# Optimization experiments

Hardware: AMD Instinct MI355X
Metric: run time of the kernel (lower is better)

Reference implementation:

```python
import jax, jax.numpy as jnp
import numpy as np

FRAME_LEN = 128
FFT_LEN = 128            # smallest power of 2 >= frame_length (TF default)
NUM_SPEC_BINS = FFT_LEN // 2 + 1  # 65
NUM_MEL = 80
SAMPLE_RATE = 16000.0
LOWER_HZ, UPPER_HZ = 80.0, 7600.0


def _hz_to_mel(f):
    # TF's HTK-style mel: 1127 * ln(1 + f/700)
    return 1127.0 * np.log1p(np.asarray(f, dtype=np.float64) / 700.0)


def _linear_to_mel_weight_matrix():
    # Faithful port of tf.signal.linear_to_mel_weight_matrix
    linear_freqs = np.linspace(0.0, SAMPLE_RATE / 2.0, NUM_SPEC_BINS)
    spec_mel = _hz_to_mel(linear_freqs[1:])[:, None]            # [64, 1] (bin 0 zeroed)
    edges = np.linspace(_hz_to_mel(LOWER_HZ), _hz_to_mel(UPPER_HZ), NUM_MEL + 2)
    lower, center, upper = edges[None, :-2], edges[None, 1:-1], edges[None, 2:]
    lower_slopes = (spec_mel - lower) / (center - lower)
    upper_slopes = (upper - spec_mel) / (upper - center)
    w = np.maximum(0.0, np.minimum(lower_slopes, upper_slopes))  # [64, 80]
    return np.pad(w, [[1, 0], [0, 0]]).astype(np.float32)        # [65, 80]


_MEL_W = jnp.asarray(_linear_to_mel_weight_matrix())


def setup_inputs() -> dict:
    key = jax.random.key(0)
    x = jax.random.normal(key, (16, 16384), dtype=jnp.float32)
    return {"x": x}


def reference(x):
    B, N = x.shape
    # pad_end=True with frame_step=1 -> N frames, pad FRAME_LEN-1 zeros at the end
    xp = jnp.pad(x, ((0, 0), (0, FRAME_LEN - 1)))
    idx = jnp.arange(N)[:, None] + jnp.arange(FRAME_LEN)[None, :]  # [N, 128]
    frames = xp[:, idx]                                            # [B, N, 128]
    n = jnp.arange(FRAME_LEN, dtype=jnp.float32)
    window = 0.5 - 0.5 * jnp.cos(2.0 * jnp.pi * n / FRAME_LEN)     # periodic Hann
    stft = jnp.fft.rfft(frames * window, n=FFT_LEN, axis=-1)       # [B, N, 65] complex
    mag = jax.lax.stop_gradient(jnp.abs(stft).astype(jnp.float32))
    mel = mag @ _MEL_W                                             # [B, N, 80]
    return jnp.concatenate([x[..., None], mel], axis=-1)           # [B, N, 81]
```

## Files before the change

### kernel.cpp

```cpp
#include <hip/hip_runtime.h>
#include <hip/hip_fp16.h>
#include <math.h>

#define B_SZ 16
#define N_SZ 16384
#define T_FR 64
#define NTHR 256
#define NMEL 80
#define NCH  81

typedef _Float16 h8  __attribute__((ext_vector_type(8)));
typedef _Float16 h4  __attribute__((ext_vector_type(4)));
typedef float    f4  __attribute__((ext_vector_type(4)));
static_assert(sizeof(h8) == 16, "h8 must be 4 VGPRs");

__device__ _Float16 g_tab[2688 * 8];

__global__ void build_tables() {
  const int u = blockIdx.x * blockDim.x + threadIdx.x;
  if (u >= 2688) return;
  const float w0 = 6.2831853071795864769f / 128.0f;
  h8 res;
  if (u < 2048) {
    const int ln = u & 63, kk = (u >> 6) & 3, pol = (u >> 8) & 1, g = u >> 9;
    const int bin = 16 * g + (ln & 15);
    const int k0  = kk * 32 + ((ln >> 4) & 3) * 8;
#pragma unroll
    for (int j = 0; j < 8; ++j) {
      const int k = k0 + j;
      const float wh = 0.5f - 0.5f * __cosf(w0 * (float)k);
      float sv, cv;
      __sincosf(w0 * (float)((bin * k) & 127), &sv, &cv);
      res[j] = (_Float16)(pol ? (-wh * sv) : (wh * cv));
    }
  } else {
    const int u2 = u - 2048;
    const int ln = u2 & 63, kkB = (u2 >> 6) & 1, jt = u2 >> 7;
    const int mj = 16 * jt + (ln & 15);
    const int b0 = kkB * 32 + ((ln >> 4) & 3) * 8;
    const float mlo = 1127.0f * logf(1.0f + 80.0f / 700.0f);
    const float mhi = 1127.0f * logf(1.0f + 7600.0f / 700.0f);
    const float dm  = (mhi - mlo) / 81.0f;
#pragma unroll
    for (int j = 0; j < 8; ++j) {
      const int bin = b0 + j;
      const float m  = 1127.0f * logf(1.0f + 125.0f * (float)bin / 700.0f);
      const float lower = mlo + dm * (float)mj;
      const float ls = (m - lower) / dm;
      const float us = (lower + 2.0f * dm - m) / dm;
      res[j] = (_Float16)fmaxf(0.0f, fminf(ls, us));
    }
  }
  ((h8*)g_tab)[u] = res;
}

__global__ __launch_bounds__(NTHR) void melspec_kernel(const float* __restrict__ x,
                                                       float* __restrict__ out) {
  __shared__ __align__(16) _Float16 xh2[184 * 8];
  __shared__ __align__(16) _Float16 magT[512 * 8];
  __shared__ float xs[64];
  __shared__ __align__(16) float stage[T_FR * NCH];

  const int tid = threadIdx.x;
  const int t0  = blockIdx.x * T_FR;
  const int b   = blockIdx.y;
  const float* xrow = x + (size_t)b * N_SZ;

  const int wv = tid >> 6;
  const int ln = tid & 63;
  const int lr = ln & 15;
  const int lg = (ln >> 4) & 3;

  if (tid < 64) xs[tid] = xrow[t0 + tid];
  if (tid < 184) {
    h8 tmp;
#pragma unroll
    for (int j = 0; j < 8; ++j) {
      const int gix = t0 + tid + j;
      tmp[j] = (_Float16)((gix < N_SZ) ? xrow[gix] : 0.0f);
    }
    *(h8*)(xh2 + tid * 8) = tmp;
  }
  const h8* tabv = (const h8*)g_tab;
  h8 aRe[4], aIm[4];
#pragma unroll
  for (int kk = 0; kk < 4; ++kk) {
    aRe[kk] = tabv[((wv * 2 + 0) * 4 + kk) * 64 + ln];
    aIm[kk] = tabv[((wv * 2 + 1) * 4 + kk) * 64 + ln];
  }
  __syncthreads();

#pragma unroll
  for (int ft = 0; ft < 4; ++ft) {
    f4 cr = {0.f, 0.f, 0.f, 0.f};
    f4 ci = {0.f, 0.f, 0.f, 0.f};
#pragma unroll
    for (int kk = 0; kk < 4; ++kk) {
      const h8 bb = *(const h8*)(xh2 + (16 * ft + 32 * kk + 8 * lg + lr) * 8);
      cr = __builtin_amdgcn_mfma_f32_16x16x32_f16(aRe[kk], bb, cr, 0, 0, 0);
      ci = __builtin_amdgcn_mfma_f32_16x16x32_f16(aIm[kk], bb, ci, 0, 0, 0);
    }
    h4 pk;
#pragma unroll
    for (int v = 0; v < 4; ++v) {
      const float re = cr[v], im = ci[v];
      pk[v] = (_Float16)sqrtf(re * re + im * im);
    }
    const int bg = 2 * wv + (lg >> 1);
    *(h4*)(magT + ((bg * 64 + 16 * ft + lr) * 8 + 4 * (lg & 1))) = pk;
  }
  h8 aW[10];
#pragma unroll
  for (int q = 0; q < 10; ++q) aW[q] = tabv[2048 + q * 64 + ln];
  __syncthreads();

  f4 acc[5];
  {
    const f4 z = {0.f, 0.f, 0.f, 0.f};
#pragma unroll
    for (int i = 0; i < 5; ++i) acc[i] = z;
  }
#pragma unroll
  for (int kkB = 0; kkB < 2; ++kkB) {
    const h8 bb = *(const h8*)(magT + ((kkB * 4 + lg) * 64 + 16 * wv + lr) * 8);
#pragma unroll
    for (int jt = 0; jt < 5; ++jt)
      acc[jt] = __builtin_amdgcn_mfma_f32_16x16x32_f16(aW[jt * 2 + kkB], bb, acc[jt], 0, 0, 0);
  }
  {
    const int fr = 16 * wv + lr;
    float* srow = stage + fr * NCH;
    if (lg == 0) srow[0] = xs[fr];
#pragma unroll
    for (int jt = 0; jt < 5; ++jt)
#pragma unroll
      for (int v = 0; v < 4; ++v)
        srow[1 + 16 * jt + 4 * lg + v] = acc[jt][v];
  }
  __syncthreads();

  float* orow = out + ((size_t)b * N_SZ + t0) * NCH;
#pragma unroll
  for (int i = 0; i < 5; ++i) {
    const int f = i * 1024 + tid * 4;
    *(float4*)(orow + f) = *(const float4*)(stage + f);
  }
  if (tid < 64) orow[5120 + tid] = stage[5120 + tid];
}

extern "C" void kernel_launch(void* const* d_in, const int* in_sizes, int n_in,
                              void* d_out, int out_size, void* d_ws, size_t ws_size,
                              hipStream_t stream) {
  const float* x = (const float*)d_in[0];
  float* out = (float*)d_out;
  hipLaunchKernelGGL(build_tables, dim3(11), dim3(256), 0, stream);
  dim3 grid(N_SZ / T_FR, B_SZ);
  dim3 block(NTHR);
  hipLaunchKernelGGL(melspec_kernel, grid, block, 0, stream, x, out);
}
```

Before: 106.3 us.

## Double frames per block and write output from per-wave staging without block barrier

Each block now processes 128 frames instead of 64, which halves the grid and amortizes the table loads and window setup over more work. The mel stage is restructured so each wave handles two 16-frame groups, staging its results in a private LDS slice and storing them straight to global memory. This removes the final block-wide barrier. The magnitude buffer gets a padded stride, which likely reduces LDS bank conflicts. The costs are higher LDS use per block and fewer blocks to spread across the GPU, which may lower occupancy.

```diff
diff --git a/kernel.cpp b/kernel.cpp
--- a/kernel.cpp
+++ b/kernel.cpp
@@ -4,10 +4,11 @@
 
 #define B_SZ 16
 #define N_SZ 16384
-#define T_FR 64
+#define T_FR 128
 #define NTHR 256
 #define NMEL 80
 #define NCH  81
+#define MAGS 129
 
 typedef _Float16 h8  __attribute__((ext_vector_type(8)));
 typedef _Float16 h4  __attribute__((ext_vector_type(4)));
@@ -56,10 +57,10 @@
 
 __global__ __launch_bounds__(NTHR) void melspec_kernel(const float* __restrict__ x,
                                                        float* __restrict__ out) {
-  __shared__ __align__(16) _Float16 xh2[184 * 8];
-  __shared__ __align__(16) _Float16 magT[512 * 8];
-  __shared__ float xs[64];
-  __shared__ __align__(16) float stage[T_FR * NCH];
+  __shared__ __align__(16) _Float16 xh2[248 * 8];
+  __shared__ __align__(16) _Float16 magT[8 * MAGS * 8];
+  __shared__ float xs[T_FR];
+  __shared__ __align__(16) float stage[4][1296];
 
   const int tid = threadIdx.x;
   const int t0  = blockIdx.x * T_FR;
@@ -71,8 +72,9 @@
   const int lr = ln & 15;
   const int lg = (ln >> 4) & 3;
 
-  if (tid < 64) xs[tid] = xrow[t0 + tid];
-  if (tid < 184) {
+  if (tid < T_FR / 4)
+    ((float4*)xs)[tid] = ((const float4*)(xrow + t0))[tid];
+  if (tid < 248) {
     h8 tmp;
 #pragma unroll
     for (int j = 0; j < 8; ++j) {
@@ -91,7 +93,7 @@
   __syncthreads();
 
 #pragma unroll
-  for (int ft = 0; ft < 4; ++ft) {
+  for (int ft = 0; ft < 8; ++ft) {
     f4 cr = {0.f, 0.f, 0.f, 0.f};
     f4 ci = {0.f, 0.f, 0.f, 0.f};
 #pragma unroll
@@ -107,45 +109,52 @@
       pk[v] = (_Float16)sqrtf(re * re + im * im);
     }
     const int bg = 2 * wv + (lg >> 1);
-    *(h4*)(magT + ((bg * 64 + 16 * ft + lr) * 8 + 4 * (lg & 1))) = pk;
+    *(h4*)(magT + ((bg * MAGS + 16 * ft + lr) * 8 + 4 * (lg & 1))) = pk;
   }
   h8 aW[10];
 #pragma unroll
   for (int q = 0; q < 10; ++q) aW[q] = tabv[2048 + q * 64 + ln];
   __syncthreads();
 
-  f4 acc[5];
-  {
-    const f4 z = {0.f, 0.f, 0.f, 0.f};
-#pragma unroll
-    for (int i = 0; i < 5; ++i) acc[i] = z;
-  }
-#pragma unroll
-  for (int kkB = 0; kkB < 2; ++kkB) {
-    const h8 bb = *(const h8*)(magT + ((kkB * 4 + lg) * 64 + 16 * wv + lr) * 8);
-#pragma unroll
-    for (int jt = 0; jt < 5; ++jt)
-      acc[jt] = __builtin_amdgcn_mfma_f32_16x16x32_f16(aW[jt * 2 + kkB], bb, acc[jt], 0, 0, 0);
-  }
-  {
-    const int fr = 16 * wv + lr;
-    float* srow = stage + fr * NCH;
-    if (lg == 0) srow[0] = xs[fr];
-#pragma unroll
-    for (int jt = 0; jt < 5; ++jt)
-#pragma unroll
-      for (int v = 0; v < 4; ++v)
-        srow[1 + 16 * jt + 4 * lg + v] = acc[jt][v];
-  }
-  __syncthreads();
-
   float* orow = out + ((size_t)b * N_SZ + t0) * NCH;
 #pragma unroll
-  for (int i = 0; i < 5; ++i) {
-    const int f = i * 1024 + tid * 4;
-    *(float4*)(orow + f) = *(const float4*)(stage + f);
+  for (int gi = 0; gi < 2; ++gi) {
+    const int g = wv + 4 * gi;
+    f4 acc[5];
+    {
+      const f4 z = {0.f, 0.f, 0.f, 0.f};
+#pragma unroll
+      for (int i = 0; i < 5; ++i) acc[i] = z;
+    }
+#pragma unroll
+    for (int kkB = 0; kkB < 2; ++kkB) {
+      const h8 bb = *(const h8*)(magT + ((kkB * 4 + lg) * MAGS + 16 * g + lr) * 8);
+#pragma unroll
+      for (int jt = 0; jt < 5; ++jt)
+        acc[jt] = __builtin_amdgcn_mfma_f32_16x16x32_f16(aW[jt * 2 + kkB], bb, acc[jt], 0, 0, 0);
+    }
+    {
+      float* srow = stage[wv] + lr * NCH;
+      if (lg == 0) srow[0] = xs[16 * g + lr];
+#pragma unroll
+      for (int jt = 0; jt < 5; ++jt)
+#pragma unroll
+        for (int v = 0; v < 4; ++v)
+          srow[1 + 16 * jt + 4 * lg + v] = acc[jt][v];
+    }
+    __asm volatile("s_waitcnt lgkmcnt(0)" ::: "memory");
+    float* obase = orow + (size_t)(16 * g) * NCH;
+    const float* sl = stage[wv];
+#pragma unroll
+    for (int i = 0; i < 5; ++i) {
+      const int f = (i * 64 + ln) * 4;
+      *(float4*)(obase + f) = *(const float4*)(sl + f);
+    }
+    if (ln < 4) {
+      const int f = (320 + ln) * 4;
+      *(float4*)(obase + f) = *(const float4*)(sl + f);
+    }
   }
-  if (tid < 64) orow[5120 + tid] = stage[5120 + tid];
 }
 
 extern "C" void kernel_launch(void* const* d_in, const int* in_sizes, int n_in,
```

Measured after the change: 102.3 us. 3.8% less time.
